# Performance work log

Measured on AMD Instinct MI355X. Metric: run time of the kernel, lower is better.

Reference implementation:

```python
import jax, jax.numpy as jnp
import numpy as np

TEMPERATURE = 1.0  # SpriteAssembler.compositing_temperature
EPS = 1e-6


def setup_inputs() -> dict:
    key = jax.random.key(0)
    k1, k2 = jax.random.split(key)
    B, H, W, N = 8, 256, 256, 64
    shapes = jax.random.uniform(k1, (B, H, W, N), dtype=jnp.float32)  # occupancy in [0,1]
    depths = jax.random.normal(k2, (B, N), dtype=jnp.float32)
    return {"shapes": shapes, "depths": depths}


def reference(shapes, depths):
    # custom_composite: depth-ordered log-space alpha compositing.
    # mask_i = s_i * prod_j (1 - s_j) ** tanh(relu((d_j - d_i)/T)), then normalize.
    d = depths / max(TEMPERATURE, 1e-6)                      # [B, N]
    s = jnp.clip(shapes, EPS, 1.0 - EPS)                     # [B, H, W, N]
    # occlusion weights: w[b, i, j] = tanh(relu(d_j - d_i))
    w = jnp.tanh(jax.nn.relu(d[:, None, :] - d[:, :, None]))  # [B, N, N]
    log1m = jnp.log1p(-s)                                    # log(1 - s), [B, H, W, N]
    # log_mask_i = log(s_i) + sum_j log(1 - s_j) * w[i, j]  (j == i term is 0 since w[i,i]=0)
    log_masks = jnp.log(s) + jnp.einsum('bhwj,bij->bhwi', log1m, w)
    unnormalized = jnp.exp(log_masks)                        # [B, H, W, N]
    masks = unnormalized / (jnp.sum(unnormalized, axis=-1, keepdims=True) + EPS)
    return masks
```

## Files before the change

kernel.cpp:

```cpp
#include <hip/hip_runtime.h>


typedef __attribute__((ext_vector_type(8))) _Float16 half8;
typedef __attribute__((ext_vector_type(4))) float floatx4;

#define EPSF 1e-6f

__device__ inline float fast_exp2(float x){ return __builtin_amdgcn_exp2f(x); }
__device__ inline float fast_log2(float x){ return __builtin_amdgcn_logf(x); }
__device__ inline float fast_rcp (float x){ return __builtin_amdgcn_rcpf(x); }

__global__ __launch_bounds__(256, 2) void sprite_mfma_kernel(
    const float* __restrict__ shapes,
    const float* __restrict__ depths,
    float* __restrict__ out)
{
    const int wave  = threadIdx.x >> 6;
    const int lane  = threadIdx.x & 63;
    const int batch = blockIdx.x >> 7;
    const int rblk  = blockIdx.x & 127;
    const int wid   = rblk * 4 + wave;

    __shared__ float dsh[64];
    __shared__ __align__(16) float ustage[4][16][68];

    if (threadIdx.x < 64) dsh[threadIdx.x] = depths[batch * 64 + threadIdx.x];
    __syncthreads();

    const int c = lane & 15;
    const int q = lane >> 4;

    half8 Aw[4][2];
    #pragma unroll
    for (int it = 0; it < 4; ++it) {
        float di = dsh[it * 16 + c];
        #pragma unroll
        for (int kt = 0; kt < 2; ++kt) {
            half8 h;
            #pragma unroll
            for (int jj = 0; jj < 8; ++jj) {
                int j = kt * 32 + q * 8 + jj;
                float x = fmaxf(dsh[j] - di, 0.0f);
                float e = fast_exp2(x * 2.885390082f);
                h[jj] = (_Float16)((e - 1.0f) * fast_rcp(e + 1.0f));
            }
            Aw[it][kt] = h;
        }
    }

    half8 idlo, idhi;
    #pragma unroll
    for (int jj = 0; jj < 8; ++jj) {
        idlo[jj] = (q * 8 + jj == c)      ? (_Float16)1.0f : (_Float16)0.0f;
        idhi[jj] = (q * 8 + jj == 16 + c) ? (_Float16)1.0f : (_Float16)0.0f;
    }

    const long pxbase = (long)batch * 65536 + (long)wid * 128;
    const float* sp = shapes + (pxbase + c) * 64 + q * 8;
    float* const obase0 = out + pxbase * 64;

    float4 pf0 = *(const float4*)(sp);
    float4 pf1 = *(const float4*)(sp + 4);
    float4 pf2 = *(const float4*)(sp + 32);
    float4 pf3 = *(const float4*)(sp + 36);

    for (int tile = 0; tile < 8; ++tile) {
        float4 s0 = pf0, s1 = pf1, s2 = pf2, s3 = pf3;
        if (tile < 7) {
            const float* sn = sp + (tile + 1) * 16 * 64;
            pf0 = *(const float4*)(sn);
            pf1 = *(const float4*)(sn + 4);
            pf2 = *(const float4*)(sn + 32);
            pf3 = *(const float4*)(sn + 36);
        }

        float sv[16] = {s0.x, s0.y, s0.z, s0.w, s1.x, s1.y, s1.z, s1.w,
                        s2.x, s2.y, s2.z, s2.w, s3.x, s3.y, s3.z, s3.w};
        half8 B_lo, B_hi;
        half8 C_lo, C_hi;
        #pragma unroll
        for (int e = 0; e < 8; ++e) {
            float slo = fminf(fmaxf(sv[e],     EPSF), 1.0f - EPSF);
            float shi = fminf(fmaxf(sv[8 + e], EPSF), 1.0f - EPSF);
            B_lo[e] = (_Float16)fast_log2(1.0f - slo);
            B_hi[e] = (_Float16)fast_log2(1.0f - shi);
            C_lo[e] = (_Float16)fast_log2(slo);
            C_hi[e] = (_Float16)fast_log2(shi);
        }

        floatx4 acc[4];
        #pragma unroll
        for (int it = 0; it < 4; ++it) {
            floatx4 a = {0.f, 0.f, 0.f, 0.f};
            a = __builtin_amdgcn_mfma_f32_16x16x32_f16(Aw[it][0], B_lo, a, 0, 0, 0);
            a = __builtin_amdgcn_mfma_f32_16x16x32_f16(Aw[it][1], B_hi, a, 0, 0, 0);
            a = __builtin_amdgcn_mfma_f32_16x16x32_f16(
                    (it & 1) ? idhi : idlo, (it < 2) ? C_lo : C_hi, a, 0, 0, 0);
            acc[it] = a;
        }

        float u[4][4];
        float tot = 0.f;
        #pragma unroll
        for (int it = 0; it < 4; ++it) {
            #pragma unroll
            for (int r = 0; r < 4; ++r) {
                float v = fast_exp2(acc[it][r]);
                u[it][r] = v;
                tot += v;
            }
        }
        tot += __shfl_xor(tot, 16, 64);
        tot += __shfl_xor(tot, 32, 64);
        float inv = fast_rcp(tot + EPSF);

        #pragma unroll
        for (int it = 0; it < 4; ++it) {
            floatx4 o = {u[it][0] * inv, u[it][1] * inv,
                         u[it][2] * inv, u[it][3] * inv};
            *(floatx4*)&ustage[wave][c][it * 16 + q * 4] = o;
        }
        float* ob = obase0 + (long)tile * 16 * 64;
        #pragma unroll
        for (int k = 0; k < 4; ++k) {
            floatx4 o = *(const floatx4*)&ustage[wave][k * 4 + q][c * 4];
            *(floatx4*)(ob + k * 256 + lane * 4) = o;
        }
    }
}

extern "C" void kernel_launch(void* const* d_in, const int* in_sizes, int n_in,
                              void* d_out, int out_size, void* d_ws, size_t ws_size,
                              hipStream_t stream) {
    const float* shapes = (const float*)d_in[0];
    const float* depths = (const float*)d_in[1];
    float* out = (float*)d_out;
    sprite_mfma_kernel<<<1024, 256, 0, stream>>>(shapes, depths, out);
}
```

Before: 234.5 us.

## Deepen shapes prefetch to two tiles with inline-asm loads and explicit vmcnt waits

Replaces the single-tile register prefetch with a two-deep ping-pong buffer (LA/LB). The buffers are filled by inline-asm global_load_dwordx4 and consumed after hand-counted s_waitcnt vmcnt waits that also account for the outstanding stores. The first two tiles' loads are issued before the tanh occlusion-weight setup so their latency overlaps that compute. The tile loop is fully unrolled through macros around a lambda. Hand-tuned vmcnt values are fragile, and the asm memory clobbers and sched barriers may limit compiler scheduling.

```diff
diff --git a/kernel.cpp b/kernel.cpp
--- a/kernel.cpp
+++ b/kernel.cpp
@@ -9,6 +9,20 @@
 __device__ inline float fast_exp2(float x){ return __builtin_amdgcn_exp2f(x); }
 __device__ inline float fast_log2(float x){ return __builtin_amdgcn_logf(x); }
 __device__ inline float fast_rcp (float x){ return __builtin_amdgcn_rcpf(x); }
+
+#define ALOAD(d0, d1, d2, d3, addr)                                           \
+    asm volatile("global_load_dwordx4 %0, %4, off\n\t"                        \
+                 "global_load_dwordx4 %1, %4, off offset:16\n\t"              \
+                 "global_load_dwordx4 %2, %4, off offset:128\n\t"             \
+                 "global_load_dwordx4 %3, %4, off offset:144"                 \
+                 : "=v"(d0), "=v"(d1), "=v"(d2), "=v"(d3)                     \
+                 : "v"(addr) : "memory")
+
+#define WAITVM(N)                                                             \
+    do {                                                                      \
+        asm volatile("s_waitcnt vmcnt(" #N ")" ::: "memory");                 \
+        __builtin_amdgcn_sched_barrier(0);                                    \
+    } while (0)
 
 __global__ __launch_bounds__(256, 2) void sprite_mfma_kernel(
     const float* __restrict__ shapes,
@@ -30,6 +44,14 @@
     const int c = lane & 15;
     const int q = lane >> 4;
 
+    const long pxbase = (long)batch * 65536 + (long)wid * 128;
+    const float* sp = shapes + (pxbase + c) * 64 + q * 8;
+    float* const obase0 = out + pxbase * 64;
+
+    floatx4 LA0, LA1, LA2, LA3, LB0, LB1, LB2, LB3;
+    ALOAD(LA0, LA1, LA2, LA3, sp);
+    ALOAD(LB0, LB1, LB2, LB3, sp + 1024);
+
     half8 Aw[4][2];
     #pragma unroll
     for (int it = 0; it < 4; ++it) {
@@ -47,7 +69,6 @@
             Aw[it][kt] = h;
         }
     }
-
     half8 idlo, idhi;
     #pragma unroll
     for (int jj = 0; jj < 8; ++jj) {
@@ -55,27 +76,9 @@
         idhi[jj] = (q * 8 + jj == 16 + c) ? (_Float16)1.0f : (_Float16)0.0f;
     }
 
-    const long pxbase = (long)batch * 65536 + (long)wid * 128;
-    const float* sp = shapes + (pxbase + c) * 64 + q * 8;
-    float* const obase0 = out + pxbase * 64;
-
-    float4 pf0 = *(const float4*)(sp);
-    float4 pf1 = *(const float4*)(sp + 4);
-    float4 pf2 = *(const float4*)(sp + 32);
-    float4 pf3 = *(const float4*)(sp + 36);
-
-    for (int tile = 0; tile < 8; ++tile) {
-        float4 s0 = pf0, s1 = pf1, s2 = pf2, s3 = pf3;
-        if (tile < 7) {
-            const float* sn = sp + (tile + 1) * 16 * 64;
-            pf0 = *(const float4*)(sn);
-            pf1 = *(const float4*)(sn + 4);
-            pf2 = *(const float4*)(sn + 32);
-            pf3 = *(const float4*)(sn + 36);
-        }
-
-        float sv[16] = {s0.x, s0.y, s0.z, s0.w, s1.x, s1.y, s1.z, s1.w,
-                        s2.x, s2.y, s2.z, s2.w, s3.x, s3.y, s3.z, s3.w};
+    auto process = [&](floatx4 s0, floatx4 s1, floatx4 s2, floatx4 s3, int tile) {
+        float sv[16] = {s0[0], s0[1], s0[2], s0[3], s1[0], s1[1], s1[2], s1[3],
+                        s2[0], s2[1], s2[2], s2[3], s3[0], s3[1], s3[2], s3[3]};
         half8 B_lo, B_hi;
         half8 C_lo, C_hi;
         #pragma unroll
@@ -126,7 +129,34 @@
             floatx4 o = *(const floatx4*)&ustage[wave][k * 4 + q][c * 4];
             *(floatx4*)(ob + k * 256 + lane * 4) = o;
         }
-    }
+    };
+
+#define TILE_A(T, NW, DOLOAD)                                                 \
+    do {                                                                      \
+        WAITVM(NW);                                                           \
+        floatx4 s0 = LA0, s1 = LA1, s2 = LA2, s3 = LA3;                       \
+        if (DOLOAD) ALOAD(LA0, LA1, LA2, LA3, sp + ((T) + 2) * 1024);         \
+        process(s0, s1, s2, s3, (T));                                         \
+    } while (0)
+#define TILE_B(T, NW, DOLOAD)                                                 \
+    do {                                                                      \
+        WAITVM(NW);                                                           \
+        floatx4 s0 = LB0, s1 = LB1, s2 = LB2, s3 = LB3;                       \
+        if (DOLOAD) ALOAD(LB0, LB1, LB2, LB3, sp + ((T) + 2) * 1024);         \
+        process(s0, s1, s2, s3, (T));                                         \
+    } while (0)
+
+    TILE_A(0,  4, 1);
+    TILE_B(1,  8, 1);
+    TILE_A(2, 12, 1);
+    TILE_B(3, 12, 1);
+    TILE_A(4, 12, 1);
+    TILE_B(5, 12, 1);
+    TILE_A(6, 12, 0);
+    TILE_B(7,  8, 0);
+
+#undef TILE_A
+#undef TILE_B
 }
 
 extern "C" void kernel_launch(void* const* d_in, const int* in_sizes, int n_in,
```

Measured after the change: 235.0 us. No clear change (+0.2%).
